# Kernel optimization log

Hardware: AMD Instinct MI355X
Metric: run time of the kernel (lower is better)

## Reference

```python
import jax, jax.numpy as jnp
import numpy as np

EOS_IDX = 2
B, LAYERS, HEADS, SEQ = 1, 33, 20, 512


def setup_inputs() -> dict:
    key = jax.random.key(0)
    k1, k2, k3, k4 = jax.random.split(key, 4)
    tokens = jax.random.randint(k1, (B, SEQ), 0, 30)
    attentions = jax.random.normal(k2, (B, LAYERS, HEADS, SEQ, SEQ), dtype=jnp.float32)
    weight = jax.random.normal(k3, (LAYERS * HEADS,), dtype=jnp.float32) * 0.05
    bias = jax.random.normal(k4, (1,), dtype=jnp.float32) * 0.05
    return {"tokens": tokens, "attentions": attentions, "weight": weight, "bias": bias}


def reference(tokens, attentions, weight, bias):
    b, nl, nh, s, _ = attentions.shape
    # mask out positions at/after EOS token pairs
    eos = (tokens != EOS_IDX).astype(attentions.dtype)           # [B, S]
    mask2d = eos[:, None, :] * eos[:, :, None]                   # [B, S, S]
    att = attentions * mask2d[:, None, None, :, :]
    # [..., :-1, :-1] then [..., 1:, 1:] == drop first and last positions
    att = att[..., 1:-1, 1:-1]                                   # [B, L, H, S-2, S-2]
    att = att.reshape(b, nl * nh, s - 2, s - 2)                  # [B, F, s2, s2]
    # symmetrize
    sym = att + jnp.swapaxes(att, -1, -2)
    # average product correction
    a1 = sym.sum(-1, keepdims=True)                              # [B, F, s2, 1]
    a2 = sym.sum(-2, keepdims=True)                              # [B, F, 1, s2]
    a12 = sym.sum((-1, -2), keepdims=True)                       # [B, F, 1, 1]
    norm = sym - a1 * a2 / a12
    logits = jnp.einsum('bfij,f->bij', norm, weight) + bias[0]
    return jax.nn.sigmoid(logits)                                # [B, s2, s2]
```

## Files before the change

kernel.cpp:

```cpp
#include <hip/hip_runtime.h>
#include <math.h>

#define SEQ   512
#define NF    660
#define CROP  510
#define EOSI  2
#define RT    16
#define GH    20
#define NT_   32
#define NG    33

typedef float f4 __attribute__((ext_vector_type(4)));

__device__ __forceinline__ f4 ntl4(const float* p) {
    return __builtin_nontemporal_load((const f4*)p);
}


#define LOADP(buf, f, prow) do {                                              \
    const float* _b = A + ((size_t)(f) << 18) + ((size_t)(prow) << 9);        \
    buf[0] = ntl4(_b + 4 * lane);                                             \
    buf[1] = ntl4(_b + 256 + 4 * lane);                                       \
    buf[2] = ntl4(_b + 512 + 4 * lane);                                       \
    buf[3] = ntl4(_b + 768 + 4 * lane);                                       \
} while (0)

#define COMP(buf, wf, cacc, wa, POFF, f) do {                                 \
    _Pragma("unroll")                                                         \
    for (int rr = 0; rr < 2; ++rr) {                                          \
        const float mi = mrow[(POFF) * 2 + rr];                               \
        f4 x0 = buf[2 * rr], x1 = buf[2 * rr + 1];                            \
        float vals[8] = {x0[0], x0[1], x0[2], x0[3],                          \
                         x1[0], x1[1], x1[2], x1[3]};                         \
        float rs = 0.f;                                                       \
        _Pragma("unroll")                                                     \
        for (int e = 0; e < 8; ++e) {                                         \
            const float v = vals[e];                                          \
            wa[rr][e] += (wf) * v;                                            \
            rs += mskv[e] * v;                                                \
            cacc[e] += mi * v;                                                \
        }                                                                     \
        _Pragma("unroll")                                                     \
        for (int off = 32; off > 0; off >>= 1)                                \
            rs += __shfl_down(rs, off, 64);                                   \
        if (lane == 0)                                                        \
            rowsum[((size_t)(f) << 9) + row0 + (POFF) * 2 + rr] = rs;         \
    }                                                                         \
} while (0)

__global__ __launch_bounds__(256) void pass1_kernel(
    const float* __restrict__ A, const int* __restrict__ tokens,
    const float* __restrict__ weight,
    float* __restrict__ WApart, float* __restrict__ rowsum, float* __restrict__ colpart)
{
    __shared__ float msk[SEQ];
    __shared__ float col_lds[2][4][2][SEQ];

    const int t = blockIdx.x, g = blockIdx.y;
    const int tid = threadIdx.x, wave = tid >> 6, lane = tid & 63;

    for (int j = tid; j < SEQ; j += 256)
        msk[j] = (j >= 1 && j <= SEQ - 2 && tokens[j] != EOSI) ? 1.f : 0.f;
    __syncthreads();

    float mskv[8];
    #pragma unroll
    for (int e = 0; e < 8; ++e)
        mskv[e] = msk[(e >> 2) * 256 + 4 * lane + (e & 3)];

    const int row0 = t * RT + wave * 4;
    const float mrow[4] = {msk[row0], msk[row0 + 1], msk[row0 + 2], msk[row0 + 3]};

    float waLo[2][8], waHi[2][8];
    #pragma unroll
    for (int r = 0; r < 2; ++r)
        #pragma unroll
        for (int e = 0; e < 8; ++e) { waLo[r][e] = 0.f; waHi[r][e] = 0.f; }

    f4 bufA[4], bufB[4];
    const int fbase = g * GH;
    LOADP(bufA, fbase, row0);

    for (int hp = 0; hp < 10; ++hp) {
        const int f0 = fbase + 2 * hp, f1 = f0 + 1;
        const float wf0 = weight[f0], wf1 = weight[f1];
        float caccA[8] = {0, 0, 0, 0, 0, 0, 0, 0};
        float caccB[8] = {0, 0, 0, 0, 0, 0, 0, 0};

        LOADP(bufB, f0, row0 + 2);
        COMP(bufA, wf0, caccA, waLo, 0, f0);
        LOADP(bufA, f1, row0);
        COMP(bufB, wf0, caccA, waHi, 1, f0);
        LOADP(bufB, f1, row0 + 2);
        COMP(bufA, wf1, caccB, waLo, 0, f1);
        if (hp < 9) LOADP(bufA, f0 + 2, row0);
        COMP(bufB, wf1, caccB, waHi, 1, f1);

        const int pp = hp & 1;
        #pragma unroll
        for (int e = 0; e < 8; ++e) {
            const int c = (e >> 2) * 256 + 4 * lane + (e & 3);
            col_lds[pp][wave][0][c] = caccA[e];
            col_lds[pp][wave][1][c] = caccB[e];
        }
        __syncthreads();
        #pragma unroll
        for (int jj = 0; jj < 4; ++jj) {
            const int j = jj * 256 + tid;
            const int h = j >> 9, c = j & 511;
            const float s = col_lds[pp][0][h][c] + col_lds[pp][1][h][c]
                          + col_lds[pp][2][h][c] + col_lds[pp][3][h][c];
            colpart[((size_t)t * NF + f0 + h) * SEQ + c] = s;
        }
    }

    float* __restrict__ wp = WApart + (size_t)g * SEQ * SEQ;
    #pragma unroll
    for (int rr = 0; rr < 2; ++rr) {
        f4 l0 = {waLo[rr][0], waLo[rr][1], waLo[rr][2], waLo[rr][3]};
        f4 l1 = {waLo[rr][4], waLo[rr][5], waLo[rr][6], waLo[rr][7]};
        *(f4*)(wp + ((size_t)(row0 + rr) << 9) + 4 * lane) = l0;
        *(f4*)(wp + ((size_t)(row0 + rr) << 9) + 256 + 4 * lane) = l1;
        f4 h0 = {waHi[rr][0], waHi[rr][1], waHi[rr][2], waHi[rr][3]};
        f4 h1 = {waHi[rr][4], waHi[rr][5], waHi[rr][6], waHi[rr][7]};
        *(f4*)(wp + ((size_t)(row0 + 2 + rr) << 9) + 4 * lane) = h0;
        *(f4*)(wp + ((size_t)(row0 + 2 + rr) << 9) + 256 + 4 * lane) = h1;
    }
}

__global__ __launch_bounds__(512) void kernel2(
    const float* __restrict__ WApart, float* __restrict__ WA,
    const float* __restrict__ rowsum, const float* __restrict__ colpart,
    const int* __restrict__ tokens, const float* __restrict__ weight,
    float* __restrict__ a1, float* __restrict__ sfac)
{
    __shared__ float part[8];
    const int b = blockIdx.x, tid = threadIdx.x;
    if (b < 128) {
        const size_t idx4 = (size_t)b * 512 + tid;
        f4 a = ntl4(WApart + 4 * idx4);
        #pragma unroll
        for (int g = 1; g < NG; ++g) {
            f4 x = ntl4(WApart + (size_t)g * (SEQ * SEQ) + 4 * idx4);
            a += x;
        }
        *(f4*)(WA + 4 * idx4) = a;
    } else {
        const int f = b - 128, j = tid;
        float cs = 0.f;
        #pragma unroll
        for (int t = 0; t < NT_; ++t)
            cs += colpart[((size_t)t * NF + f) * SEQ + j];
        const float m = (j >= 1 && j <= SEQ - 2 && tokens[j] != EOSI) ? 1.f : 0.f;
        const float v = m * (rowsum[((size_t)f << 9) + j] + cs);
        a1[((size_t)f << 9) + j] = v;
        float s = v;
        #pragma unroll
        for (int off = 32; off > 0; off >>= 1)
            s += __shfl_down(s, off, 64);
        const int wave = tid >> 6, lane = tid & 63;
        if (lane == 0) part[wave] = s;
        __syncthreads();
        if (tid == 0) {
            float a12 = 0.f;
            #pragma unroll
            for (int k = 0; k < 8; ++k) a12 += part[k];
            sfac[f] = weight[f] / a12;
        }
    }
}

__global__ __launch_bounds__(256) void pass3_kernel(
    const float* __restrict__ WA, const float* __restrict__ a1,
    const float* __restrict__ sfac, const int* __restrict__ tokens,
    const float* __restrict__ bias, float* __restrict__ out)
{
    const int TI = blockIdx.y * 32;
    const int TJ = blockIdx.x * 32;
    const int tid = threadIdx.x;
    const int tx = tid & 15, ty = tid >> 4;

    __shared__ float u_s[16][33];
    __shared__ float v_s[16][33];

    float acc[2][2] = {{0.f, 0.f}, {0.f, 0.f}};

    for (int f0 = 0; f0 < NF; f0 += 16) {
        for (int e = tid; e < 512; e += 256) {
            const int ff = e >> 5, ii = e & 31;
            const int f = f0 + ff;
            int Iu = TI + 1 + ii; if (Iu > SEQ - 1) Iu = SEQ - 1;
            int Ju = TJ + 1 + ii; if (Ju > SEQ - 1) Ju = SEQ - 1;
            if (f < NF) {
                u_s[ff][ii] = a1[(size_t)f * SEQ + Iu] * sfac[f];
                v_s[ff][ii] = a1[(size_t)f * SEQ + Ju];
            } else {
                u_s[ff][ii] = 0.0f;
                v_s[ff][ii] = 0.0f;
            }
        }
        __syncthreads();
        #pragma unroll
        for (int ff = 0; ff < 16; ++ff) {
            const float u0 = u_s[ff][2 * ty],     u1 = u_s[ff][2 * ty + 1];
            const float w0 = v_s[ff][2 * tx],     w1 = v_s[ff][2 * tx + 1];
            acc[0][0] += u0 * w0; acc[0][1] += u0 * w1;
            acc[1][0] += u1 * w0; acc[1][1] += u1 * w1;
        }
        __syncthreads();
    }

    const float b = bias[0];
    #pragma unroll
    for (int dy = 0; dy < 2; ++dy) {
        #pragma unroll
        for (int dx = 0; dx < 2; ++dx) {
            const int i = TI + 2 * ty + dy;
            const int j = TJ + 2 * tx + dx;
            if (i < CROP && j < CROP) {
                const int I = i + 1, J = j + 1;
                const float mi = (tokens[I] != EOSI) ? 1.0f : 0.0f;
                const float mj = (tokens[J] != EOSI) ? 1.0f : 0.0f;
                const float first = mi * mj * (WA[(size_t)I * SEQ + J] + WA[(size_t)J * SEQ + I]);
                const float logit = first - acc[dy][dx] + b;
                out[(size_t)i * CROP + j] = 1.0f / (1.0f + expf(-logit));
            }
        }
    }
}

extern "C" void kernel_launch(void* const* d_in, const int* in_sizes, int n_in,
                              void* d_out, int out_size, void* d_ws, size_t ws_size,
                              hipStream_t stream) {
    const int*   tokens = (const int*)d_in[0];
    const float* A      = (const float*)d_in[1];
    const float* weight = (const float*)d_in[2];
    const float* bias   = (const float*)d_in[3];
    float* out = (float*)d_out;

    float* WApart  = (float*)d_ws;
    float* colpart = WApart + (size_t)NG * SEQ * SEQ;
    float* WA      = colpart + (size_t)NT_ * NF * SEQ;
    float* rowsum  = WA + (size_t)SEQ * SEQ;
    float* a1      = rowsum + (size_t)NF * SEQ;
    float* sfac    = a1 + (size_t)NF * SEQ;

    dim3 g1(NT_, NG);
    pass1_kernel<<<g1, 256, 0, stream>>>(A, tokens, weight, WApart, rowsum, colpart);

    kernel2<<<128 + NF, 512, 0, stream>>>(WApart, WA, rowsum, colpart, tokens, weight, a1, sfac);

    dim3 g3(16, 16);
    pass3_kernel<<<g3, 256, 0, stream>>>(WA, a1, sfac, tokens, bias, out);
}
```

Measured before the change: 227.6 us.

## Rebalance pass1 feature groups to 32 and shrink pass3 tiles to 16x16

Pass1 now uses 32 feature groups instead of 33. Twenty groups take 21 features and the rest take 20, with a tail step for the extra feature, so the grid is 32x32 blocks and should fill the CUs more evenly. It also adds a minimum-occupancy launch bound. Pass3 switches from 32x32 tiles with 2x2 outputs per thread to 16x16 tiles with one output per thread over 32-feature chunks, quadrupling the block count for more parallelism at the cost of more redundant a1 loads.

```diff
diff --git a/kernel.cpp b/kernel.cpp
--- a/kernel.cpp
+++ b/kernel.cpp
@@ -6,16 +6,14 @@
 #define CROP  510
 #define EOSI  2
 #define RT    16
-#define GH    20
 #define NT_   32
-#define NG    33
+#define NG    32
 
 typedef float f4 __attribute__((ext_vector_type(4)));
 
 __device__ __forceinline__ f4 ntl4(const float* p) {
     return __builtin_nontemporal_load((const f4*)p);
 }
-
 
 #define LOADP(buf, f, prow) do {                                              \
     const float* _b = A + ((size_t)(f) << 18) + ((size_t)(prow) << 9);        \
@@ -48,7 +46,7 @@
     }                                                                         \
 } while (0)
 
-__global__ __launch_bounds__(256) void pass1_kernel(
+__global__ __launch_bounds__(256, 4) void pass1_kernel(
     const float* __restrict__ A, const int* __restrict__ tokens,
     const float* __restrict__ weight,
     float* __restrict__ WApart, float* __restrict__ rowsum, float* __restrict__ colpart)
@@ -59,6 +57,9 @@
     const int t = blockIdx.x, g = blockIdx.y;
     const int tid = threadIdx.x, wave = tid >> 6, lane = tid & 63;
 
+    const int f0   = (g < 20) ? 21 * g : 420 + 20 * (g - 20);
+    const int tail = (g < 20) ? 1 : 0;
+
     for (int j = tid; j < SEQ; j += 256)
         msk[j] = (j >= 1 && j <= SEQ - 2 && tokens[j] != EOSI) ? 1.f : 0.f;
     __syncthreads();
@@ -78,23 +79,23 @@
         for (int e = 0; e < 8; ++e) { waLo[r][e] = 0.f; waHi[r][e] = 0.f; }
 
     f4 bufA[4], bufB[4];
-    const int fbase = g * GH;
-    LOADP(bufA, fbase, row0);
+    LOADP(bufA, f0, row0);
 
     for (int hp = 0; hp < 10; ++hp) {
-        const int f0 = fbase + 2 * hp, f1 = f0 + 1;
-        const float wf0 = weight[f0], wf1 = weight[f1];
+        const int fa = f0 + 2 * hp, fb = fa + 1;
+        const float wf0 = weight[fa], wf1 = weight[fb];
         float caccA[8] = {0, 0, 0, 0, 0, 0, 0, 0};
         float caccB[8] = {0, 0, 0, 0, 0, 0, 0, 0};
 
-        LOADP(bufB, f0, row0 + 2);
-        COMP(bufA, wf0, caccA, waLo, 0, f0);
-        LOADP(bufA, f1, row0);
-        COMP(bufB, wf0, caccA, waHi, 1, f0);
-        LOADP(bufB, f1, row0 + 2);
-        COMP(bufA, wf1, caccB, waLo, 0, f1);
-        if (hp < 9) LOADP(bufA, f0 + 2, row0);
-        COMP(bufB, wf1, caccB, waHi, 1, f1);
+        LOADP(bufB, fa, row0 + 2);
+        COMP(bufA, wf0, caccA, waLo, 0, fa);
+        LOADP(bufA, fb, row0);
+        COMP(bufB, wf0, caccA, waHi, 1, fa);
+        LOADP(bufB, fb, row0 + 2);
+        COMP(bufA, wf1, caccB, waLo, 0, fb);
+        if (hp < 9)       LOADP(bufA, fa + 2, row0);
+        else if (tail)    LOADP(bufA, f0 + 20, row0);
+        COMP(bufB, wf1, caccB, waHi, 1, fb);
 
         const int pp = hp & 1;
         #pragma unroll
@@ -108,9 +109,29 @@
         for (int jj = 0; jj < 4; ++jj) {
             const int j = jj * 256 + tid;
             const int h = j >> 9, c = j & 511;
-            const float s = col_lds[pp][0][h][c] + col_lds[pp][1][h][c]
-                          + col_lds[pp][2][h][c] + col_lds[pp][3][h][c];
-            colpart[((size_t)t * NF + f0 + h) * SEQ + c] = s;
+            colpart[((size_t)t * NF + fa + h) * SEQ + c] =
+                col_lds[pp][0][h][c] + col_lds[pp][1][h][c]
+              + col_lds[pp][2][h][c] + col_lds[pp][3][h][c];
+        }
+    }
+
+    if (tail) {
+        const int ft = f0 + 20;
+        const float wft = weight[ft];
+        float caccA[8] = {0, 0, 0, 0, 0, 0, 0, 0};
+        LOADP(bufB, ft, row0 + 2);
+        COMP(bufA, wft, caccA, waLo, 0, ft);
+        COMP(bufB, wft, caccA, waHi, 1, ft);
+        #pragma unroll
+        for (int e = 0; e < 8; ++e)
+            col_lds[0][wave][0][(e >> 2) * 256 + 4 * lane + (e & 3)] = caccA[e];
+        __syncthreads();
+        #pragma unroll
+        for (int jj = 0; jj < 2; ++jj) {
+            const int c = jj * 256 + tid;
+            colpart[((size_t)t * NF + ft) * SEQ + c] =
+                col_lds[0][0][0][c] + col_lds[0][1][0][c]
+              + col_lds[0][2][0][c] + col_lds[0][3][0][c];
         }
     }
 
@@ -175,57 +196,49 @@
     const float* __restrict__ sfac, const int* __restrict__ tokens,
     const float* __restrict__ bias, float* __restrict__ out)
 {
-    const int TI = blockIdx.y * 32;
-    const int TJ = blockIdx.x * 32;
+    const int TI = blockIdx.y * 16;
+    const int TJ = blockIdx.x * 16;
     const int tid = threadIdx.x;
     const int tx = tid & 15, ty = tid >> 4;
 
-    __shared__ float u_s[16][33];
-    __shared__ float v_s[16][33];
-
-    float acc[2][2] = {{0.f, 0.f}, {0.f, 0.f}};
-
-    for (int f0 = 0; f0 < NF; f0 += 16) {
-        for (int e = tid; e < 512; e += 256) {
-            const int ff = e >> 5, ii = e & 31;
+    __shared__ float u_s[32][17];
+    __shared__ float v_s[32][17];
+
+    float acc = 0.f;
+
+    for (int f0 = 0; f0 < NF; f0 += 32) {
+        #pragma unroll
+        for (int c = 0; c < 4; ++c) {
+            const int e = c * 256 + tid;
+            const int arr = e >> 9, ff = (e >> 4) & 31, ii = e & 15;
             const int f = f0 + ff;
-            int Iu = TI + 1 + ii; if (Iu > SEQ - 1) Iu = SEQ - 1;
-            int Ju = TJ + 1 + ii; if (Ju > SEQ - 1) Ju = SEQ - 1;
+            float val = 0.f;
             if (f < NF) {
-                u_s[ff][ii] = a1[(size_t)f * SEQ + Iu] * sfac[f];
-                v_s[ff][ii] = a1[(size_t)f * SEQ + Ju];
-            } else {
-                u_s[ff][ii] = 0.0f;
-                v_s[ff][ii] = 0.0f;
+                if (arr == 0) {
+                    int Iu = TI + 1 + ii; if (Iu > SEQ - 1) Iu = SEQ - 1;
+                    val = a1[((size_t)f << 9) + Iu] * sfac[f];
+                } else {
+                    int Ju = TJ + 1 + ii; if (Ju > SEQ - 1) Ju = SEQ - 1;
+                    val = a1[((size_t)f << 9) + Ju];
+                }
             }
-        }
-        __syncthreads();
-        #pragma unroll
-        for (int ff = 0; ff < 16; ++ff) {
-            const float u0 = u_s[ff][2 * ty],     u1 = u_s[ff][2 * ty + 1];
-            const float w0 = v_s[ff][2 * tx],     w1 = v_s[ff][2 * tx + 1];
-            acc[0][0] += u0 * w0; acc[0][1] += u0 * w1;
-            acc[1][0] += u1 * w0; acc[1][1] += u1 * w1;
-        }
-        __syncthreads();
-    }
-
-    const float b = bias[0];
-    #pragma unroll
-    for (int dy = 0; dy < 2; ++dy) {
-        #pragma unroll
-        for (int dx = 0; dx < 2; ++dx) {
-            const int i = TI + 2 * ty + dy;
-            const int j = TJ + 2 * tx + dx;
-            if (i < CROP && j < CROP) {
-                const int I = i + 1, J = j + 1;
-                const float mi = (tokens[I] != EOSI) ? 1.0f : 0.0f;
-                const float mj = (tokens[J] != EOSI) ? 1.0f : 0.0f;
-                const float first = mi * mj * (WA[(size_t)I * SEQ + J] + WA[(size_t)J * SEQ + I]);
-                const float logit = first - acc[dy][dx] + b;
-                out[(size_t)i * CROP + j] = 1.0f / (1.0f + expf(-logit));
-            }
-        }
+            if (arr == 0) u_s[ff][ii] = val; else v_s[ff][ii] = val;
+        }
+        __syncthreads();
+        #pragma unroll
+        for (int ff = 0; ff < 32; ++ff)
+            acc += u_s[ff][ty] * v_s[ff][tx];
+        __syncthreads();
+    }
+
+    const int i = TI + ty, j = TJ + tx;
+    if (i < CROP && j < CROP) {
+        const int I = i + 1, J = j + 1;
+        const float mi = (tokens[I] != EOSI) ? 1.f : 0.f;
+        const float mj = (tokens[J] != EOSI) ? 1.f : 0.f;
+        const float first = mi * mj * (WA[((size_t)I << 9) + J] + WA[((size_t)J << 9) + I]);
+        const float logit = first - acc + bias[0];
+        out[(size_t)i * CROP + j] = 1.f / (1.f + expf(-logit));
     }
 }
 
@@ -250,6 +263,6 @@
 
     kernel2<<<128 + NF, 512, 0, stream>>>(WApart, WA, rowsum, colpart, tokens, weight, a1, sfac);
 
-    dim3 g3(16, 16);
+    dim3 g3(32, 32);
     pass3_kernel<<<g3, 256, 0, stream>>>(WA, a1, sfac, tokens, bias, out);
 }
```

After: 249.1 us. 9.4% more time.
